# Kernel optimization log

Measured on AMD Instinct MI355X. Metric: run time of the kernel, lower is better.

Reference implementation:

```python
import jax, jax.numpy as jnp
import numpy as np

DIM = 512
HEADS = 8
DIM_HEAD = 64
INNER = HEADS * DIM_HEAD


def setup_inputs() -> dict:
    key = jax.random.key(0)
    k1, k2, k3, k4 = jax.random.split(key, 4)
    x = jax.random.normal(k1, (4, 8192, DIM), dtype=jnp.float32)
    # nn.Linear(dim, inner*3, bias=False): weight applied as x @ W^T; store transposed form [dim, 3*inner]
    w_qkv = jax.random.normal(k2, (DIM, 3 * INNER), dtype=jnp.float32) / np.sqrt(DIM)
    w_out = jax.random.normal(k3, (INNER, DIM), dtype=jnp.float32) / np.sqrt(INNER)
    b_out = jax.random.normal(k4, (DIM,), dtype=jnp.float32) * 0.01
    return {"x": x, "w_qkv": w_qkv, "w_out": w_out, "b_out": b_out}


def reference(x, w_qkv, w_out, b_out):
    b, n, d = x.shape
    qkv = x @ w_qkv  # [b, n, 3*inner]
    q, k, v = jnp.split(qkv, 3, axis=-1)

    def to_heads(t):
        return t.reshape(b, n, HEADS, DIM_HEAD).transpose(0, 2, 1, 3)  # [b,h,n,dh]

    q, k, v = map(to_heads, (q, k, v))
    q = jax.nn.elu(q) + 1.0
    k = jax.nn.elu(k) + 1.0
    # kv summary: [b,h,dh,dh]
    kv = jnp.einsum('bhnd,bhnm->bhdm', k, v)
    # normalizer z: [b,h,n]  (note: original does NOT apply self.scale)
    z = 1.0 / (jnp.einsum('bhnd,bhd->bhn', q, k.sum(axis=2)) + 1e-6)
    out = jnp.einsum('bhnd,bhdm->bhnm', q, kv) * z[..., None]  # [b,h,n,dh]
    out = out.transpose(0, 2, 1, 3).reshape(b, n, INNER)
    return out @ w_out + b_out
```

## Files before the change

kernel.cpp:

```cpp
#include <hip/hip_runtime.h>
#include <hip/hip_bf16.h>

#define B_SZ 4
#define SEQ 8192
#define DIM 512
#define HEADS 8
#define DH 64
#define INNER 512
#define QKV_COLS 1536
#define M_TOT (B_SZ * SEQ)
#define BHN (B_SZ * HEADS)

typedef __bf16 bf16x8 __attribute__((ext_vector_type(8)));
typedef __bf16 bf16x4 __attribute__((ext_vector_type(4)));
typedef float f32x4 __attribute__((ext_vector_type(4)));

__device__ __forceinline__ float elu1(float x) {
    return x > 0.f ? x + 1.f : __expf(x);
}

__device__ __forceinline__ void gl_lds16(const void* g, void* l) {
    __builtin_amdgcn_global_load_lds(
        (const __attribute__((address_space(1))) unsigned int*)g,
        (__attribute__((address_space(3))) unsigned int*)l, 16, 0, 0);
}

#define MFMA16(a, b, c) __builtin_amdgcn_mfma_f32_16x16x32_bf16(a, b, c, 0, 0, 0)

__global__ void convert_all(const float* __restrict__ x,
                            const float* __restrict__ w_qkv,
                            const float* __restrict__ w_out,
                            __bf16* __restrict__ xb,
                            __bf16* __restrict__ wqkv_t,
                            __bf16* __restrict__ wout_t) {
    const int NX = M_TOT * DIM / 4;
    int id = blockIdx.x * 256 + threadIdx.x;
    if (id < NX) {
        float4 f = reinterpret_cast<const float4*>(x)[id];
        bf16x4 h = {(__bf16)f.x, (__bf16)f.y, (__bf16)f.z, (__bf16)f.w};
        reinterpret_cast<bf16x4*>(xb)[id] = h;
        return;
    }
    int id2 = id - NX;
    if (id2 < QKV_COLS * DIM) {
        int n = id2 / DIM, k = id2 % DIM;
        wqkv_t[id2] = (__bf16)w_qkv[k * QKV_COLS + n];
    } else {
        int id3 = id2 - QKV_COLS * DIM;
        if (id3 < INNER * DIM) {
            int n = id3 / DIM, k = id3 % DIM;
            wout_t[id3] = (__bf16)w_out[k * DIM + n];
        }
    }
}

#define TSTR 136
__launch_bounds__(256, 2)
__global__ void gemm_qkv(const __bf16* __restrict__ xb,
                         const __bf16* __restrict__ wqkv_t,
                         __bf16* __restrict__ q_ws,
                         __bf16* __restrict__ kT_ws,
                         __bf16* __restrict__ vT_ws) {
    __shared__ __attribute__((aligned(16))) char smem[128 * TSTR * 2];
    __bf16* As = (__bf16*)smem;
    __bf16* Bs = (__bf16*)(smem + 16384);
    __bf16* T  = (__bf16*)smem;

    const int tid = threadIdx.x;
    const int wid = tid >> 6;
    const int lane = tid & 63;
    const int wm = wid >> 1, wn = wid & 1;
    const int lq = lane >> 4, lr = lane & 15;
    const int m0 = blockIdx.x * 128;
    const int n0 = blockIdx.y * 128;
    const int lrow = lane >> 3;
    const int lsw  = ((lane & 7) ^ lrow) * 8;

    f32x4 acc[4][4] = {};

    for (int kb = 0; kb < DIM; kb += 64) {
#pragma unroll
        for (int t = 0; t < 4; ++t) {
            int qi = wid * 4 + t;
            int row = qi * 8 + lrow;
            gl_lds16(&xb[(size_t)(m0 + row) * DIM + kb + lsw], &As[qi * 512]);
            gl_lds16(&wqkv_t[(size_t)(n0 + row) * DIM + kb + lsw], &Bs[qi * 512]);
        }
        __syncthreads();
#pragma unroll
        for (int ks = 0; ks < 2; ++ks) {
            const int csw = ((ks * 4 + lq) ^ (lr & 7)) * 8;
            bf16x8 af[4], bfv[4];
#pragma unroll
            for (int i = 0; i < 4; ++i)
                af[i] = *reinterpret_cast<const bf16x8*>(
                    &As[(wm * 64 + i * 16 + lr) * 64 + csw]);
#pragma unroll
            for (int j = 0; j < 4; ++j)
                bfv[j] = *reinterpret_cast<const bf16x8*>(
                    &Bs[(wn * 64 + j * 16 + lr) * 64 + csw]);
#pragma unroll
            for (int i = 0; i < 4; ++i)
#pragma unroll
                for (int j = 0; j < 4; ++j)
                    acc[i][j] = MFMA16(af[i], bfv[j], acc[i][j]);
        }
        __syncthreads();
    }

    const int which = n0 / INNER;
    const int n0w = n0 % INNER;
    const int b = m0 / SEQ;
    const int nbase = m0 % SEQ;

    if (which == 0) {
#pragma unroll
        for (int i = 0; i < 4; ++i)
#pragma unroll
            for (int j = 0; j < 4; ++j) {
                int col = wn * 64 + j * 16 + lr;
#pragma unroll
                for (int r = 0; r < 4; ++r)
                    T[(wm * 64 + i * 16 + lq * 4 + r) * TSTR + col] =
                        (__bf16)elu1(acc[i][j][r]);
            }
        __syncthreads();
#pragma unroll
        for (int it = 0; it < 8; ++it) {
            int c = tid + it * 256;
            int row = c >> 4, dc = (c & 15) * 8;
            bf16x8 v = *reinterpret_cast<const bf16x8*>(&T[row * TSTR + dc]);
            int col = n0w + dc;
            int h = col >> 6, d = col & 63;
            *reinterpret_cast<bf16x8*>(
                &q_ws[(((size_t)(b * HEADS + h)) * SEQ + nbase + row) * DH + d]) = v;
        }
    } else {
        __bf16* dst = (which == 1) ? kT_ws : vT_ws;
#pragma unroll
        for (int i = 0; i < 4; ++i)
#pragma unroll
            for (int j = 0; j < 4; ++j) {
                int col = wn * 64 + j * 16 + lr;
                int rowb = wm * 64 + i * 16 + lq * 4;
                bf16x4 h4;
#pragma unroll
                for (int r = 0; r < 4; ++r) {
                    float v = acc[i][j][r];
                    h4[r] = (__bf16)((which == 1) ? elu1(v) : v);
                }
                *reinterpret_cast<bf16x4*>(&T[col * TSTR + rowb]) = h4;
            }
        __syncthreads();
#pragma unroll
        for (int it = 0; it < 8; ++it) {
            int c = tid + it * 256;
            int colIdx = c >> 4, rc = (c & 15) * 8;
            bf16x8 v = *reinterpret_cast<const bf16x8*>(&T[colIdx * TSTR + rc]);
            int gcol = n0w + colIdx;
            int h = gcol >> 6, d = gcol & 63;
            *reinterpret_cast<bf16x8*>(
                &dst[(((size_t)(b * HEADS + h)) * DH + d) * SEQ + nbase + rc]) = v;
        }
    }
}

__launch_bounds__(256, 2)
__global__ void kv_reduce(const __bf16* __restrict__ kT,
                          const __bf16* __restrict__ vT,
                          float* __restrict__ kv_t,
                          float* __restrict__ ksum) {
    __shared__ __attribute__((aligned(16))) __bf16 Ks[64][136];
    __shared__ __attribute__((aligned(16))) __bf16 Vs[64][136];
    const int tid = threadIdx.x;
    const int wid = tid >> 6;
    const int lane = tid & 63;
    const int lq = lane >> 4, lr = lane & 15;
    const int bh = blockIdx.y;
    const int n0 = blockIdx.x * 512;
    const size_t base = (size_t)bh * DH * SEQ;
    f32x4 acc[4] = {};
    f32x4 acc1 = {};
    bf16x8 ones8;
#pragma unroll
    for (int e = 0; e < 8; ++e) ones8[e] = (__bf16)1.f;

    for (int ch = 0; ch < 4; ++ch) {
        int nc = n0 + ch * 128;
#pragma unroll
        for (int t = 0; t < 4; ++t) {
            int c = tid + t * 256;
            int row = c >> 4, kc = (c & 15) * 8;
            *reinterpret_cast<bf16x8*>(&Ks[row][kc]) =
                *reinterpret_cast<const bf16x8*>(&kT[base + (size_t)row * SEQ + nc + kc]);
            *reinterpret_cast<bf16x8*>(&Vs[row][kc]) =
                *reinterpret_cast<const bf16x8*>(&vT[base + (size_t)row * SEQ + nc + kc]);
        }
        __syncthreads();
#pragma unroll
        for (int ks = 0; ks < 4; ++ks) {
            bf16x8 a = *reinterpret_cast<const bf16x8*>(&Ks[wid * 16 + lr][ks * 32 + lq * 8]);
            acc1 = MFMA16(a, ones8, acc1);
#pragma unroll
            for (int j = 0; j < 4; ++j) {
                bf16x8 b = *reinterpret_cast<const bf16x8*>(&Vs[j * 16 + lr][ks * 32 + lq * 8]);
                acc[j] = MFMA16(a, b, acc[j]);
            }
        }
        __syncthreads();
    }
    float* dst = kv_t + (size_t)bh * DH * DH;
#pragma unroll
    for (int j = 0; j < 4; ++j) {
        int m = j * 16 + lr;
#pragma unroll
        for (int r = 0; r < 4; ++r) {
            int d = wid * 16 + lq * 4 + r;
            atomicAdd(&dst[m * DH + d], acc[j][r]);
        }
    }
    if (lr == 0) {
#pragma unroll
        for (int r = 0; r < 4; ++r)
            atomicAdd(&ksum[bh * DH + wid * 16 + lq * 4 + r], acc1[r]);
    }
}

__launch_bounds__(512, 2)
__global__ void attn_out(const __bf16* __restrict__ q_ws,
                         const float* __restrict__ kv_t,
                         const float* __restrict__ ksum,
                         const __bf16* __restrict__ wout_t,
                         const float* __restrict__ b_out,
                         float* __restrict__ out) {
    __shared__ __attribute__((aligned(16))) __bf16 kvs[2][64 * 64];
    __shared__ __attribute__((aligned(16))) __bf16 attn_lds[128 * 64];
    __shared__ float zs[128];

    const int tid = threadIdx.x;
    const int wid = tid >> 6, lane = tid & 63;
    const int lq = lane >> 4, lr = lane & 15;
    const int wm = wid >> 2, wn = wid & 3;
    const int m0 = blockIdx.x * 128;
    const int b = m0 / SEQ;
    const int nseq = m0 % SEQ;

    f32x4 acc[4][8] = {};

    auto stage_kv = [&](int buf, int h) {
        int m = tid >> 3, c0 = tid & 7;
        const float* src = &kv_t[(((size_t)(b * 8 + h)) * 64 + m) * 64 + c0 * 8];
        float4 f0 = *reinterpret_cast<const float4*>(src);
        float4 f1 = *reinterpret_cast<const float4*>(src + 4);
        bf16x8 v = {(__bf16)f0.x, (__bf16)f0.y, (__bf16)f0.z, (__bf16)f0.w,
                    (__bf16)f1.x, (__bf16)f1.y, (__bf16)f1.z, (__bf16)f1.w};
        *reinterpret_cast<bf16x8*>(&kvs[buf][m * 64 + ((c0 ^ (m & 7)) * 8)]) = v;
    };

    stage_kv(0, 0);
    __syncthreads();

    for (int h = 0; h < 8; ++h) {
        const int buf = h & 1;
        const size_t qb = (((size_t)(b * 8 + h)) * SEQ + nseq) * DH;

        {
            int row = tid >> 2, part = tid & 3;
            const __bf16* qp = &q_ws[qb + (size_t)row * DH + part * 16];
            bf16x8 v0 = *reinterpret_cast<const bf16x8*>(qp);
            bf16x8 v1 = *reinterpret_cast<const bf16x8*>(qp + 8);
            const float* kp = &ksum[(b * 8 + h) * 64 + part * 16];
            float s = 0.f;
#pragma unroll
            for (int j = 0; j < 8; ++j) s += (float)v0[j] * kp[j];
#pragma unroll
            for (int j = 0; j < 8; ++j) s += (float)v1[j] * kp[8 + j];
            s += __shfl_xor(s, 1, 64);
            s += __shfl_xor(s, 2, 64);
            if (part == 0) zs[row] = 1.f / (s + 1e-6f);
        }

        {
            const int r0 = wid * 16;
            bf16x8 qa[2];
#pragma unroll
            for (int ks = 0; ks < 2; ++ks)
                qa[ks] = *reinterpret_cast<const bf16x8*>(
                    &q_ws[qb + (size_t)(r0 + lr) * DH + ks * 32 + lq * 8]);
            f32x4 acc1[4] = {};
#pragma unroll
            for (int ks = 0; ks < 2; ++ks)
#pragma unroll
                for (int j = 0; j < 4; ++j) {
                    int mr = j * 16 + lr;
                    bf16x8 bk = *reinterpret_cast<const bf16x8*>(
                        &kvs[buf][mr * 64 + (((ks * 4 + lq) ^ (mr & 7)) * 8)]);
                    acc1[j] = MFMA16(qa[ks], bk, acc1[j]);
                }
            asm volatile("s_waitcnt lgkmcnt(0)" ::: "memory");
            float zr[4];
#pragma unroll
            for (int r = 0; r < 4; ++r) zr[r] = zs[r0 + lq * 4 + r];
#pragma unroll
            for (int j = 0; j < 4; ++j)
#pragma unroll
                for (int r = 0; r < 4; ++r) {
                    int row = r0 + lq * 4 + r;
                    int chk = j * 2 + (lr >> 3);
                    attn_lds[row * 64 + ((chk ^ (row & 7)) * 8) + (lr & 7)] =
                        (__bf16)(acc1[j][r] * zr[r]);
                }
        }
        if (h < 7) stage_kv(buf ^ 1, h + 1);
        __syncthreads();

        {
            bf16x8 af[4][2];
#pragma unroll
            for (int i = 0; i < 4; ++i)
#pragma unroll
                for (int ks = 0; ks < 2; ++ks) {
                    int arow = wm * 64 + i * 16 + lr;
                    af[i][ks] = *reinterpret_cast<const bf16x8*>(
                        &attn_lds[arow * 64 + (((ks * 4 + lq) ^ (arow & 7)) * 8)]);
                }
#pragma unroll
            for (int n = 0; n < 8; ++n) {
                int c = wn * 128 + n * 16 + lr;
                const __bf16* wp = &wout_t[(size_t)c * 512 + h * 64 + lq * 8];
                bf16x8 bw0 = *reinterpret_cast<const bf16x8*>(wp);
                bf16x8 bw1 = *reinterpret_cast<const bf16x8*>(wp + 32);
                __builtin_amdgcn_s_setprio(1);
#pragma unroll
                for (int i = 0; i < 4; ++i) {
                    acc[i][n] = MFMA16(af[i][0], bw0, acc[i][n]);
                    acc[i][n] = MFMA16(af[i][1], bw1, acc[i][n]);
                }
                __builtin_amdgcn_s_setprio(0);
            }
        }
        __syncthreads();
    }

#pragma unroll
    for (int n = 0; n < 8; ++n) {
        int col = wn * 128 + n * 16 + lr;
        float bias = b_out[col];
#pragma unroll
        for (int i = 0; i < 4; ++i) {
            int row = m0 + wm * 64 + i * 16 + lq * 4;
#pragma unroll
            for (int r = 0; r < 4; ++r)
                out[(size_t)(row + r) * DIM + col] = acc[i][n][r] + bias;
        }
    }
}

extern "C" void kernel_launch(void* const* d_in, const int* in_sizes, int n_in,
                              void* d_out, int out_size, void* d_ws, size_t ws_size,
                              hipStream_t stream) {
    (void)in_sizes; (void)n_in; (void)out_size; (void)ws_size;
    const float* x     = (const float*)d_in[0];
    const float* w_qkv = (const float*)d_in[1];
    const float* w_out = (const float*)d_in[2];
    const float* b_out = (const float*)d_in[3];
    float* out = (float*)d_out;

    char* ws = (char*)d_ws;
    size_t off = 0;
    auto alloc = [&](size_t bytes) {
        char* p = ws + off;
        off += (bytes + 255) & ~(size_t)255;
        return p;
    };
    __bf16* xb     = (__bf16*)alloc((size_t)M_TOT * DIM * 2);
    __bf16* q_ws   = (__bf16*)alloc((size_t)BHN * SEQ * DH * 2);
    __bf16* kT_ws  = (__bf16*)alloc((size_t)BHN * SEQ * DH * 2);
    __bf16* vT_ws  = (__bf16*)alloc((size_t)BHN * SEQ * DH * 2);
    float*  kv_t   = (float*)alloc((size_t)BHN * DH * DH * 4 + (size_t)BHN * DH * 4);
    float*  ksum   = kv_t + (size_t)BHN * DH * DH;
    __bf16* wqkv_t = (__bf16*)alloc((size_t)QKV_COLS * DIM * 2);
    __bf16* wout_t = (__bf16*)alloc((size_t)INNER * DIM * 2);

    hipMemsetAsync(kv_t, 0, (size_t)BHN * DH * DH * 4 + (size_t)BHN * DH * 4, stream);
    convert_all<<<dim3(M_TOT * DIM / 4 / 256 + (QKV_COLS * DIM + INNER * DIM) / 256),
                  256, 0, stream>>>(x, w_qkv, w_out, xb, wqkv_t, wout_t);
    gemm_qkv<<<dim3(M_TOT / 128, QKV_COLS / 128), 256, 0, stream>>>(
        xb, wqkv_t, q_ws, kT_ws, vT_ws);
    kv_reduce<<<dim3(16, BHN), 256, 0, stream>>>(kT_ws, vT_ws, kv_t, ksum);
    attn_out<<<dim3(M_TOT / 128), 512, 0, stream>>>(
        q_ws, kv_t, ksum, wout_t, b_out, out);
}
```

Measured before the change: 293.7 us.

## Remap QKV GEMM blocks per XCD and shrink attn_out tiles to 64 rows

The QKV GEMM block index is remapped so that consecutive blocks on the same XCD (blockIdx mod 8) share M rows across all 12 N tiles, which should improve L2 reuse of x tiles. attn_out moves from 128-row tiles with 512 threads to 64-row tiles with 256 threads, doubling the grid. Each wave now covers all 64 rows and 128 output columns. W_out fragment loads are batched four at a time before the MFMAs to give more memory-level parallelism. The trade-off is that W_out and kv staging traffic per output row doubles, and the MFMA loop uses more registers.

After: 290.5 us. No clear change (-1.1%).

```diff
diff --git a/kernel.cpp b/kernel.cpp
--- a/kernel.cpp
+++ b/kernel.cpp
@@ -71,8 +71,11 @@
     const int lane = tid & 63;
     const int wm = wid >> 1, wn = wid & 1;
     const int lq = lane >> 4, lr = lane & 15;
-    const int m0 = blockIdx.x * 128;
-    const int n0 = blockIdx.y * 128;
+    const int f  = blockIdx.y * gridDim.x + blockIdx.x;
+    const int xc = f & 7, sl = f >> 3;
+    const int ml = sl / 12, nn = sl % 12;
+    const int m0 = (xc * 32 + ml) * 128;
+    const int n0 = nn * 128;
     const int lrow = lane >> 3;
     const int lsw  = ((lane & 7) ^ lrow) * 8;
 
@@ -226,7 +229,7 @@
     }
 }
 
-__launch_bounds__(512, 2)
+__launch_bounds__(256, 2)
 __global__ void attn_out(const __bf16* __restrict__ q_ws,
                          const float* __restrict__ kv_t,
                          const float* __restrict__ ksum,
@@ -234,27 +237,31 @@
                          const float* __restrict__ b_out,
                          float* __restrict__ out) {
     __shared__ __attribute__((aligned(16))) __bf16 kvs[2][64 * 64];
-    __shared__ __attribute__((aligned(16))) __bf16 attn_lds[128 * 64];
-    __shared__ float zs[128];
+    __shared__ __attribute__((aligned(16))) __bf16 attn_lds[64 * 64];
+    __shared__ float zs[64];
 
     const int tid = threadIdx.x;
     const int wid = tid >> 6, lane = tid & 63;
     const int lq = lane >> 4, lr = lane & 15;
-    const int wm = wid >> 2, wn = wid & 3;
-    const int m0 = blockIdx.x * 128;
+    const int wn = wid;
+    const int m0 = blockIdx.x * 64;
     const int b = m0 / SEQ;
     const int nseq = m0 % SEQ;
 
     f32x4 acc[4][8] = {};
 
     auto stage_kv = [&](int buf, int h) {
-        int m = tid >> 3, c0 = tid & 7;
+        int m = tid >> 2, c0 = (tid & 3) * 2;
         const float* src = &kv_t[(((size_t)(b * 8 + h)) * 64 + m) * 64 + c0 * 8];
-        float4 f0 = *reinterpret_cast<const float4*>(src);
-        float4 f1 = *reinterpret_cast<const float4*>(src + 4);
-        bf16x8 v = {(__bf16)f0.x, (__bf16)f0.y, (__bf16)f0.z, (__bf16)f0.w,
-                    (__bf16)f1.x, (__bf16)f1.y, (__bf16)f1.z, (__bf16)f1.w};
-        *reinterpret_cast<bf16x8*>(&kvs[buf][m * 64 + ((c0 ^ (m & 7)) * 8)]) = v;
+#pragma unroll
+        for (int u = 0; u < 2; ++u) {
+            float4 f0 = *reinterpret_cast<const float4*>(src + u * 8);
+            float4 f1 = *reinterpret_cast<const float4*>(src + u * 8 + 4);
+            bf16x8 v = {(__bf16)f0.x, (__bf16)f0.y, (__bf16)f0.z, (__bf16)f0.w,
+                        (__bf16)f1.x, (__bf16)f1.y, (__bf16)f1.z, (__bf16)f1.w};
+            *reinterpret_cast<bf16x8*>(
+                &kvs[buf][m * 64 + (((c0 + u) ^ (m & 7)) * 8)]) = v;
+        }
     };
 
     stage_kv(0, 0);
@@ -320,22 +327,28 @@
             for (int i = 0; i < 4; ++i)
 #pragma unroll
                 for (int ks = 0; ks < 2; ++ks) {
-                    int arow = wm * 64 + i * 16 + lr;
+                    int arow = i * 16 + lr;
                     af[i][ks] = *reinterpret_cast<const bf16x8*>(
                         &attn_lds[arow * 64 + (((ks * 4 + lq) ^ (arow & 7)) * 8)]);
                 }
 #pragma unroll
-            for (int n = 0; n < 8; ++n) {
-                int c = wn * 128 + n * 16 + lr;
-                const __bf16* wp = &wout_t[(size_t)c * 512 + h * 64 + lq * 8];
-                bf16x8 bw0 = *reinterpret_cast<const bf16x8*>(wp);
-                bf16x8 bw1 = *reinterpret_cast<const bf16x8*>(wp + 32);
+            for (int half = 0; half < 2; ++half) {
+                bf16x8 bw[4][2];
+#pragma unroll
+                for (int nn = 0; nn < 4; ++nn) {
+                    int c = wn * 128 + (half * 4 + nn) * 16 + lr;
+                    const __bf16* wp = &wout_t[(size_t)c * 512 + h * 64 + lq * 8];
+                    bw[nn][0] = *reinterpret_cast<const bf16x8*>(wp);
+                    bw[nn][1] = *reinterpret_cast<const bf16x8*>(wp + 32);
+                }
                 __builtin_amdgcn_s_setprio(1);
 #pragma unroll
-                for (int i = 0; i < 4; ++i) {
-                    acc[i][n] = MFMA16(af[i][0], bw0, acc[i][n]);
-                    acc[i][n] = MFMA16(af[i][1], bw1, acc[i][n]);
-                }
+                for (int nn = 0; nn < 4; ++nn)
+#pragma unroll
+                    for (int i = 0; i < 4; ++i) {
+                        acc[i][half * 4 + nn] = MFMA16(af[i][0], bw[nn][0], acc[i][half * 4 + nn]);
+                        acc[i][half * 4 + nn] = MFMA16(af[i][1], bw[nn][1], acc[i][half * 4 + nn]);
+                    }
                 __builtin_amdgcn_s_setprio(0);
             }
         }
@@ -348,7 +361,7 @@
         float bias = b_out[col];
 #pragma unroll
         for (int i = 0; i < 4; ++i) {
-            int row = m0 + wm * 64 + i * 16 + lq * 4;
+            int row = m0 + i * 16 + lq * 4;
 #pragma unroll
             for (int r = 0; r < 4; ++r)
                 out[(size_t)(row + r) * DIM + col] = acc[i][n][r] + bias;
@@ -388,6 +401,6 @@
     gemm_qkv<<<dim3(M_TOT / 128, QKV_COLS / 128), 256, 0, stream>>>(
         xb, wqkv_t, q_ws, kT_ws, vT_ws);
     kv_reduce<<<dim3(16, BHN), 256, 0, stream>>>(kT_ws, vT_ws, kv_t, ksum);
-    attn_out<<<dim3(M_TOT / 128), 512, 0, stream>>>(
+    attn_out<<<dim3(M_TOT / 64), 256, 0, stream>>>(
         q_ws, kv_t, ksum, wout_t, b_out, out);
 }
```
